# Kernel tuning notes

Measured on AMD Instinct MI355X. Metric: run time of the kernel, lower is better.

Reference implementation:

```python
import jax, jax.numpy as jnp
import numpy as np

N = 50000      # nodes
E = 800000     # edges
H, C = 4, 32   # heads, per-head channels
NF = 513       # n_fft//2 + 1 frequency bins
NMEL = 128
NEG_SLOPE_ATT = 0.2   # GATConv leaky_relu slope
NEG_SLOPE_MLP = 0.01  # F.leaky_relu default


def setup_inputs() -> dict:
    key = jax.random.key(0)
    ks = jax.random.split(key, 12)
    s = 0.05
    return {
        "x": jax.random.normal(ks[0], (N, NF), jnp.float32),
        "edge_index": jax.random.randint(ks[1], (2, E), 0, N, dtype=jnp.int32),
        "fb": jax.random.normal(ks[2], (NF, NMEL), jnp.float32) * s,
        "Wg": jax.random.normal(ks[3], (NMEL, H * C), jnp.float32) * s,
        "bias_g": jnp.zeros((H * C,), jnp.float32),
        "att_src": jax.random.normal(ks[4], (H, C), jnp.float32) * s,
        "att_dst": jax.random.normal(ks[5], (H, C), jnp.float32) * s,
        "W1": jax.random.normal(ks[6], (H * C, 256), jnp.float32) * s,
        "b1": jnp.zeros((256,), jnp.float32),
        "W2": jax.random.normal(ks[7], (256, 128), jnp.float32) * s,
        "b2": jnp.zeros((128,), jnp.float32),
        "W3": jax.random.normal(ks[8], (128, 10), jnp.float32) * s,
        "b3": jnp.zeros((10,), jnp.float32),
    }


def gat_conv(h, src, dst, att_src, att_dst, bias_g):
    # h: [N, H, C]; per-edge attention, segment softmax over dst, scatter-add
    a_s = jnp.einsum('nhc,hc->nh', h, att_src)  # [N, H]
    a_d = jnp.einsum('nhc,hc->nh', h, att_dst)  # [N, H]
    e = jax.nn.leaky_relu(a_s[src] + a_d[dst], NEG_SLOPE_ATT)  # [E', H]
    m = jax.ops.segment_max(e, dst, num_segments=N)            # [N, H]
    ex = jnp.exp(e - m[dst])
    denom = jax.ops.segment_sum(ex, dst, num_segments=N)       # [N, H]
    alpha = ex / denom[dst]                                    # [E', H]
    msg = h[src] * alpha[:, :, None]                           # [E', H, C]
    out = jax.ops.segment_sum(msg, dst, num_segments=N)        # [N, H, C]
    return out.reshape(N, H * C) + bias_g


def reference(x, edge_index, fb, Wg, bias_g, att_src, att_dst, W1, b1, W2, b2, W3, b3):
    # learnable mel filterbank projection: [N, NF] -> [N, NMEL]
    x = x @ fb
    # GATConv linear transform, split into heads
    h = (x @ Wg).reshape(N, H, C)
    # add self loops (PyG GATConv default add_self_loops=True)
    loop = jnp.arange(N, dtype=edge_index.dtype)
    src = jnp.concatenate([edge_index[0], loop])
    dst = jnp.concatenate([edge_index[1], loop])
    x = jax.nn.elu(gat_conv(h, src, dst, att_src, att_dst, bias_g))
    # dropout is identity in eval mode
    x = jax.nn.leaky_relu(x @ W1 + b1, NEG_SLOPE_MLP)
    x = jax.nn.leaky_relu(x @ W2 + b2, NEG_SLOPE_MLP)
    x = jax.nn.leaky_relu(x @ W3 + b3, NEG_SLOPE_MLP)
    return jax.nn.softmax(x, axis=-1)
```

## Files before the change

### kernel.cpp

```cpp
#include <hip/hip_runtime.h>
#include <hip/hip_bf16.h>

#define NN 50000
#define EE 800000
#define NFR 513
#define NMEL 128
#define HC 128

typedef __bf16 bf16x8 __attribute__((ext_vector_type(8)));
typedef float floatx4 __attribute__((ext_vector_type(4)));

__device__ __forceinline__ unsigned short f2b(float f) {
    unsigned u = __float_as_uint(f);
    u = (u + 0x7FFFu + ((u >> 16) & 1u)) >> 16;
    return (unsigned short)u;
}
__device__ __forceinline__ float b2f(unsigned short s) {
    return __uint_as_float(((unsigned)s) << 16);
}
__device__ __forceinline__ float lexp(float a) {
    a = a > 0.f ? a : 0.2f * a;
    return __expf(a);
}

__device__ __forceinline__ float ldf(const float* p, long i) { return p[i]; }
__device__ __forceinline__ void stf(float* p, long i, float v) { p[i] = v; }
__device__ __forceinline__ void stf(__hip_bfloat16* p, long i, float v) {
    ((unsigned short*)p)[i] = f2b(v);
}

#define BM 64
#define BN 64
#define BK 16

template<int EPI, typename TA, typename TB, typename TC>
__global__ __launch_bounds__(256) void gemm_k(const TA* __restrict__ A, const TB* __restrict__ B,
                                              TC* __restrict__ C, int M, int Nn, int K,
                                              const float* __restrict__ bias)
{
    __shared__ float As[BK][BM + 4];
    __shared__ float Bs[BK][BN + 4];
    const int t = threadIdx.x;
    const int row0 = blockIdx.x * BM;
    const int col0 = blockIdx.y * BN;
    const int tc = t & 15, tr = t >> 4;
    float acc[4][4] = {};

    for (int kb = 0; kb < K; kb += BK) {
        #pragma unroll
        for (int i = 0; i < 4; ++i) {
            int idx = i * 256 + t;
            int r = idx >> 4, k = idx & 15;
            int gr = row0 + r, gk = kb + k;
            float v = 0.f;
            if (gr < M && gk < K) v = ldf(A, (long)gr * K + gk);
            As[k][r] = v;
        }
        #pragma unroll
        for (int i = 0; i < 4; ++i) {
            int idx = i * 256 + t;
            int c = idx & 63, k = idx >> 6;
            int gk = kb + k, gc = col0 + c;
            float v = 0.f;
            if (gk < K && gc < Nn) v = ldf(B, (long)gk * Nn + gc);
            Bs[k][c] = v;
        }
        __syncthreads();
        #pragma unroll
        for (int kk = 0; kk < BK; ++kk) {
            float4 av = *reinterpret_cast<const float4*>(&As[kk][tr << 2]);
            float4 bv = *reinterpret_cast<const float4*>(&Bs[kk][tc << 2]);
            float a[4] = {av.x, av.y, av.z, av.w};
            float b[4] = {bv.x, bv.y, bv.z, bv.w};
            #pragma unroll
            for (int i = 0; i < 4; ++i)
                #pragma unroll
                for (int j = 0; j < 4; ++j)
                    acc[i][j] += a[i] * b[j];
        }
        __syncthreads();
    }

    #pragma unroll
    for (int i = 0; i < 4; ++i) {
        int gr = row0 + (tr << 2) + i;
        if (gr >= M) continue;
        #pragma unroll
        for (int j = 0; j < 4; ++j) {
            int gc = col0 + (tc << 2) + j;
            if (gc >= Nn) continue;
            float v = acc[i][j];
            if (EPI == 2) {
                stf(C, (long)gc * 544 + gr, v);
            } else {
                if (EPI == 1) { v += bias[gc]; v = v > 0.f ? v : 0.01f * v; }
                stf(C, (long)gr * Nn + gc, v);
            }
        }
    }
}

__global__ void k_trans(const float* __restrict__ in, __hip_bfloat16* __restrict__ outp,
                        int K, int N, int KP)
{
    int id = blockIdx.x * 256 + threadIdx.x;
    if (id >= N * KP) return;
    int n = id / KP, k = id % KP;
    float v = (k < K) ? in[(long)k * N + n] : 0.f;
    ((unsigned short*)outp)[id] = f2b(v);
}

#define PS 40

template<typename T> struct ARegs;
template<> struct ARegs<float> { float v[8]; };
template<> struct ARegs<__hip_bfloat16> { uint4 v; };

__device__ __forceinline__ void loadA_r(const float* __restrict__ A, ARegs<float>& r, int t,
                                        int row0, int M, int K, int kb)
{
    #pragma unroll
    for (int g = 0; g < 2; ++g) {
        int q = g * 256 + t;
        int row = q >> 3, k4 = (q & 7) * 4;
        int gr = row0 + row, gk = kb + k4;
        float f0 = 0.f, f1 = 0.f, f2 = 0.f, f3 = 0.f;
        if (gr < M) {
            const float* ap = A + (long)gr * K + gk;
            if (gk + 3 < K) {
                f0 = ap[0]; f1 = ap[1]; f2 = ap[2]; f3 = ap[3];
            } else {
                if (gk + 0 < K) f0 = ap[0];
                if (gk + 1 < K) f1 = ap[1];
                if (gk + 2 < K) f2 = ap[2];
            }
        }
        r.v[g * 4 + 0] = f0; r.v[g * 4 + 1] = f1;
        r.v[g * 4 + 2] = f2; r.v[g * 4 + 3] = f3;
    }
}

__device__ __forceinline__ void writeA_r(unsigned short* As, const ARegs<float>& r, int t)
{
    #pragma unroll
    for (int g = 0; g < 2; ++g) {
        int q = g * 256 + t;
        int row = q >> 3, k4 = (q & 7) * 4;
        ushort4 pk;
        pk.x = f2b(r.v[g * 4 + 0]); pk.y = f2b(r.v[g * 4 + 1]);
        pk.z = f2b(r.v[g * 4 + 2]); pk.w = f2b(r.v[g * 4 + 3]);
        *reinterpret_cast<ushort4*>(&As[row * PS + k4]) = pk;
    }
}

__device__ __forceinline__ void loadA_r(const __hip_bfloat16* __restrict__ A, ARegs<__hip_bfloat16>& r,
                                        int t, int row0, int M, int K, int kb)
{
    int row = t >> 2, k8 = (t & 3) * 8;
    int gr = row0 + row;
    uint4 val = make_uint4(0, 0, 0, 0);
    if (gr < M) val = *reinterpret_cast<const uint4*>(A + (long)gr * K + kb + k8);
    r.v = val;
}

__device__ __forceinline__ void writeA_r(unsigned short* As, const ARegs<__hip_bfloat16>& r, int t)
{
    int row = t >> 2, k8 = (t & 3) * 8;
    *reinterpret_cast<uint4*>(&As[row * PS + k8]) = r.v;
}

__device__ __forceinline__ void loadB_r(const __hip_bfloat16* __restrict__ Bt, uint4* bR, int t,
                                        int col0, int Nn, int KB, int kb)
{
    #pragma unroll
    for (int g = 0; g < 2; ++g) {
        int c = g * 256 + t;
        int row = c >> 2, k8 = (c & 3) * 8;
        int gn = col0 + row;
        uint4 val = make_uint4(0, 0, 0, 0);
        if (gn < Nn) val = *reinterpret_cast<const uint4*>(Bt + (long)gn * KB + kb + k8);
        bR[g] = val;
    }
}

__device__ __forceinline__ void writeB_r(unsigned short* Bs, const uint4* bR, int t)
{
    #pragma unroll
    for (int g = 0; g < 2; ++g) {
        int c = g * 256 + t;
        int row = c >> 2, k8 = (c & 3) * 8;
        *reinterpret_cast<uint4*>(&Bs[row * PS + k8]) = bR[g];
    }
}

template<int EPI, typename TA, typename TC>
__global__ __launch_bounds__(256) void mgemm(const TA* __restrict__ A,
                                             const __hip_bfloat16* __restrict__ Bt,
                                             TC* __restrict__ C,
                                             int M, int Nn, int K, int KB,
                                             const float* __restrict__ bias)
{
    __shared__ unsigned short As[2][64 * PS];
    __shared__ unsigned short Bs[2][128 * PS];
    const int t = threadIdx.x;
    const int row0 = blockIdx.x * 64;
    const int col0 = blockIdx.y * 128;
    const int wave = t >> 6, lane = t & 63;
    const int wm = (wave >> 1) * 32, wn = (wave & 1) * 64;
    const int lm = lane & 15, kq = lane >> 4;

    floatx4 acc[2][4];
    #pragma unroll
    for (int i = 0; i < 2; ++i)
        #pragma unroll
        for (int j = 0; j < 4; ++j)
            acc[i][j] = 0.f;

    ARegs<TA> aR;
    uint4 bR[2];
    loadA_r(A, aR, t, row0, M, K, 0);
    loadB_r(Bt, bR, t, col0, Nn, KB, 0);

    const int nIter = KB >> 5;
    int b = 0;
    for (int it = 0; it < nIter; ++it) {
        writeA_r(As[b], aR, t);
        writeB_r(Bs[b], bR, t);
        if (it + 1 < nIter) {
            loadA_r(A, aR, t, row0, M, K, (it + 1) * 32);
            loadB_r(Bt, bR, t, col0, Nn, KB, (it + 1) * 32);
        }
        asm volatile("s_waitcnt lgkmcnt(0)" ::: "memory");
        __builtin_amdgcn_s_barrier();
        __builtin_amdgcn_sched_barrier(0);

        bf16x8 af[2], bf[4];
        #pragma unroll
        for (int i = 0; i < 2; ++i)
            af[i] = *reinterpret_cast<const bf16x8*>(&As[b][(wm + i * 16 + lm) * PS + kq * 8]);
        #pragma unroll
        for (int j = 0; j < 4; ++j)
            bf[j] = *reinterpret_cast<const bf16x8*>(&Bs[b][(wn + j * 16 + lm) * PS + kq * 8]);
        #pragma unroll
        for (int i = 0; i < 2; ++i)
            #pragma unroll
            for (int j = 0; j < 4; ++j)
                acc[i][j] = __builtin_amdgcn_mfma_f32_16x16x32_bf16(af[i], bf[j], acc[i][j], 0, 0, 0);
        b ^= 1;
    }

    #pragma unroll
    for (int i = 0; i < 2; ++i) {
        #pragma unroll
        for (int r = 0; r < 4; ++r) {
            int gr = row0 + wm + i * 16 + kq * 4 + r;
            if (gr >= M) continue;
            #pragma unroll
            for (int j = 0; j < 4; ++j) {
                int gc = col0 + wn + j * 16 + lm;
                float v = acc[i][j][r];
                if (EPI == 1) { v += bias[gc]; v = v > 0.f ? v : 0.01f * v; }
                stf(C, (long)gr * Nn + gc, v);
            }
        }
    }
}

__global__ void k_att(const __hip_bfloat16* __restrict__ h, const float* __restrict__ att_src,
                      const float* __restrict__ att_dst,
                      float* __restrict__ a_s, float* __restrict__ a_d)
{
    int id = blockIdx.x * blockDim.x + threadIdx.x;
    if (id >= NN * 4) return;
    int n = id >> 2, hh = id & 3;
    const unsigned short* hr = (const unsigned short*)(h + (long)n * HC + hh * 32);
    float s1 = 0.f, s2 = 0.f;
    #pragma unroll
    for (int c = 0; c < 32; ++c) {
        float v = b2f(hr[c]);
        s1 += v * att_src[hh * 32 + c];
        s2 += v * att_dst[hh * 32 + c];
    }
    a_s[id] = s1;
    a_d[id] = s2;
}

__global__ void k_hist(const int* __restrict__ ei, int* __restrict__ hist)
{
    int e = blockIdx.x * 256 + threadIdx.x;
    if (e < EE) atomicAdd(&hist[ei[EE + e]], 1);
}

__global__ __launch_bounds__(512) void k_scan1(const int* __restrict__ hist, int* __restrict__ start,
                                               int* __restrict__ aux)
{
    __shared__ int sm[512];
    int t = threadIdx.x, i = blockIdx.x * 512 + t;
    int v = (i < NN) ? hist[i] : 0;
    sm[t] = v;
    __syncthreads();
    for (int off = 1; off < 512; off <<= 1) {
        int x = (t >= off) ? sm[t - off] : 0;
        __syncthreads();
        sm[t] += x;
        __syncthreads();
    }
    if (i < NN) start[i] = sm[t] - v;
    if (t == 511) aux[blockIdx.x] = sm[511];
}

__global__ void k_scan2(int* __restrict__ aux, int nb)
{
    if (blockIdx.x == 0 && threadIdx.x == 0) {
        int run = 0;
        for (int b = 0; b < nb; ++b) { int v = aux[b]; aux[b] = run; run += v; }
    }
}

__global__ __launch_bounds__(512) void k_scan3(int* __restrict__ start, int* __restrict__ cursor,
                                               const int* __restrict__ aux)
{
    int i = blockIdx.x * 512 + threadIdx.x;
    if (i < NN) {
        int v = start[i] + aux[blockIdx.x];
        start[i] = v;
        cursor[i] = v;
    }
    if (i == 0) start[NN] = EE;
}

__global__ void k_fill(const int* __restrict__ ei, int* __restrict__ cursor, int* __restrict__ sorted)
{
    int e = blockIdx.x * 256 + threadIdx.x;
    if (e >= EE) return;
    int s = ei[e], d = ei[EE + e];
    int pos = atomicAdd(&cursor[d], 1);
    sorted[pos] = s;
}

__global__ __launch_bounds__(256) void k_agg(const int* __restrict__ start, const int* __restrict__ sorted,
                                             const float* __restrict__ a_s, const float* __restrict__ a_d,
                                             const __hip_bfloat16* __restrict__ h,
                                             const float* __restrict__ bias_g,
                                             __hip_bfloat16* __restrict__ agg)
{
    int wave = threadIdx.x >> 6;
    int lane = threadIdx.x & 63;
    int d = blockIdx.x * 4 + wave;
    if (d >= NN) return;
    int hh = lane >> 4;
    float ad = a_d[d * 4 + hh];
    int e0 = start[d], e1 = start[d + 1];

    float ex = lexp(a_s[d * 4 + hh] + ad);
    unsigned hv = *reinterpret_cast<const unsigned*>(h + (long)d * HC + 2 * lane);
    float acc0 = ex * __uint_as_float(hv << 16);
    float acc1 = ex * __uint_as_float(hv & 0xffff0000u);
    float dsum = ex;

    int e = e0;
    for (; e + 4 <= e1; e += 4) {
        int s0 = sorted[e + 0], s1 = sorted[e + 1], s2 = sorted[e + 2], s3 = sorted[e + 3];
        float as0 = a_s[s0 * 4 + hh], as1 = a_s[s1 * 4 + hh];
        float as2 = a_s[s2 * 4 + hh], as3 = a_s[s3 * 4 + hh];
        unsigned h0 = *reinterpret_cast<const unsigned*>(h + (long)s0 * HC + 2 * lane);
        unsigned h1 = *reinterpret_cast<const unsigned*>(h + (long)s1 * HC + 2 * lane);
        unsigned h2 = *reinterpret_cast<const unsigned*>(h + (long)s2 * HC + 2 * lane);
        unsigned h3 = *reinterpret_cast<const unsigned*>(h + (long)s3 * HC + 2 * lane);
        float x0 = lexp(as0 + ad), x1 = lexp(as1 + ad), x2 = lexp(as2 + ad), x3 = lexp(as3 + ad);
        acc0 += x0 * __uint_as_float(h0 << 16);
        acc1 += x0 * __uint_as_float(h0 & 0xffff0000u);
        acc0 += x1 * __uint_as_float(h1 << 16);
        acc1 += x1 * __uint_as_float(h1 & 0xffff0000u);
        acc0 += x2 * __uint_as_float(h2 << 16);
        acc1 += x2 * __uint_as_float(h2 & 0xffff0000u);
        acc0 += x3 * __uint_as_float(h3 << 16);
        acc1 += x3 * __uint_as_float(h3 & 0xffff0000u);
        dsum += x0 + x1 + x2 + x3;
    }
    for (; e < e1; ++e) {
        int s = sorted[e];
        float xe = lexp(a_s[s * 4 + hh] + ad);
        unsigned hs = *reinterpret_cast<const unsigned*>(h + (long)s * HC + 2 * lane);
        acc0 += xe * __uint_as_float(hs << 16);
        acc1 += xe * __uint_as_float(hs & 0xffff0000u);
        dsum += xe;
    }

    float inv = 1.f / dsum;
    float2 bg = *reinterpret_cast<const float2*>(bias_g + 2 * lane);
    float v0 = acc0 * inv + bg.x;
    float v1 = acc1 * inv + bg.y;
    v0 = v0 > 0.f ? v0 : expm1f(v0);
    v1 = v1 > 0.f ? v1 : expm1f(v1);
    unsigned pk = (unsigned)f2b(v0) | ((unsigned)f2b(v1) << 16);
    *reinterpret_cast<unsigned*>((unsigned short*)agg + (long)d * HC + 2 * lane) = pk;
}

__global__ __launch_bounds__(256) void k_final(const __hip_bfloat16* __restrict__ x2, const float* __restrict__ W3,
                                               const float* __restrict__ b3, float* __restrict__ out)
{
    __shared__ float w3s[128 * 10];
    __shared__ float b3s[10];
    int t = threadIdx.x;
    for (int i = t; i < 128 * 10; i += 256) w3s[i] = W3[i];
    if (t < 10) b3s[t] = b3[t];
    __syncthreads();
    int n = blockIdx.x * 256 + t;
    if (n >= NN) return;

    float l[10];
    #pragma unroll
    for (int j = 0; j < 10; ++j) l[j] = b3s[j];
    const uint4* row = reinterpret_cast<const uint4*>(x2 + (long)n * 128);
    #pragma unroll 4
    for (int c8 = 0; c8 < 16; ++c8) {
        uint4 v = row[c8];
        const unsigned w[4] = {v.x, v.y, v.z, v.w};
        #pragma unroll
        for (int u = 0; u < 4; ++u) {
            float f0 = __uint_as_float(w[u] << 16);
            float f1 = __uint_as_float(w[u] & 0xffff0000u);
            const float* wr = &w3s[(c8 * 8 + u * 2) * 10];
            #pragma unroll
            for (int j = 0; j < 10; ++j) l[j] += f0 * wr[j] + f1 * wr[10 + j];
        }
    }
    float m = -1e30f;
    #pragma unroll
    for (int j = 0; j < 10; ++j) {
        float v = l[j];
        v = v > 0.f ? v : 0.01f * v;
        l[j] = v;
        m = fmaxf(m, v);
    }
    float sum = 0.f;
    #pragma unroll
    for (int j = 0; j < 10; ++j) { l[j] = __expf(l[j] - m); sum += l[j]; }
    float inv = 1.f / sum;
    #pragma unroll
    for (int j = 0; j < 10; ++j) out[(long)n * 10 + j] = l[j] * inv;
}

extern "C" void kernel_launch(void* const* d_in, const int* in_sizes, int n_in,
                              void* d_out, int out_size, void* d_ws, size_t ws_size,
                              hipStream_t stream)
{
    const float* x       = (const float*)d_in[0];
    const int*   ei      = (const int*)d_in[1];
    const float* fb      = (const float*)d_in[2];
    const float* Wg      = (const float*)d_in[3];
    const float* bias_g  = (const float*)d_in[4];
    const float* att_src = (const float*)d_in[5];
    const float* att_dst = (const float*)d_in[6];
    const float* W1      = (const float*)d_in[7];
    const float* b1      = (const float*)d_in[8];
    const float* W2      = (const float*)d_in[9];
    const float* b2      = (const float*)d_in[10];
    const float* W3      = (const float*)d_in[11];
    const float* b3      = (const float*)d_in[12];
    float* out = (float*)d_out;
    float* ws = (float*)d_ws;

    float* a_s = ws + 0;
    float* a_d = ws + 200000;
    __hip_bfloat16* fbWgT = (__hip_bfloat16*)(ws + 400000);
    __hip_bfloat16* W1T   = (__hip_bfloat16*)(ws + 434816);
    __hip_bfloat16* W2T   = (__hip_bfloat16*)(ws + 451200);
    int* hist   = (int*)(ws + 467584);
    int* startA = (int*)(ws + 517584);
    int* aux    = (int*)(ws + 567588);
    int* sorted = (int*)(ws + 567720);
    __hip_bfloat16* hbufB = (__hip_bfloat16*)(ws + 1367720);
    __hip_bfloat16* aggB  = (__hip_bfloat16*)(ws + 4567720);
    __hip_bfloat16* x1B   = (__hip_bfloat16*)(ws + 7767720);
    int* cursor = hist;
    __hip_bfloat16* x2B = hbufB;
    if (ws_size < (size_t)14167720 * sizeof(float)) return;

    hipMemsetAsync(ws + 400000, 0, (size_t)117584 * sizeof(float), stream);

    gemm_k<2, float, float, __hip_bfloat16><<<dim3(9, 2), 256, 0, stream>>>(fb, Wg, fbWgT, NFR, HC, NMEL, nullptr);
    k_trans<<<128, 256, 0, stream>>>(W1, W1T, 128, 256, 128);
    k_trans<<<128, 256, 0, stream>>>(W2, W2T, 256, 128, 256);

    mgemm<0, float, __hip_bfloat16><<<dim3(782, 1), 256, 0, stream>>>(x, fbWgT, hbufB, NN, HC, NFR, 544, nullptr);

    k_att<<<(NN * 4 + 255) / 256, 256, 0, stream>>>(hbufB, att_src, att_dst, a_s, a_d);

    k_hist<<<(EE + 255) / 256, 256, 0, stream>>>(ei, hist);
    k_scan1<<<98, 512, 0, stream>>>(hist, startA, aux);
    k_scan2<<<1, 64, 0, stream>>>(aux, 98);
    k_scan3<<<98, 512, 0, stream>>>(startA, cursor, aux);
    k_fill<<<(EE + 255) / 256, 256, 0, stream>>>(ei, cursor, sorted);

    k_agg<<<(NN + 3) / 4, 256, 0, stream>>>(startA, sorted, a_s, a_d, hbufB, bias_g, aggB);

    mgemm<1, __hip_bfloat16, __hip_bfloat16><<<dim3(782, 2), 256, 0, stream>>>(aggB, W1T, x1B, NN, 256, 128, 128, b1);

    mgemm<1, __hip_bfloat16, __hip_bfloat16><<<dim3(782, 1), 256, 0, stream>>>(x1B, W2T, x2B, NN, 128, 256, 256, b2);

    k_final<<<(NN + 255) / 256, 256, 0, stream>>>(x2B, W3, b3, out);
}
```

Before: 429.6 us.

## Add dedicated first GEMM keeping whole B tile in LDS and loading A directly

Replaces the generic double-buffered GEMM for the x @ (fb·Wg) projection with a specialised kernel of 512 threads and 128-row blocks. Half of the transposed B matrix is staged in shared memory per phase, while each wave reads its fp32 A rows straight from global memory into registers, converts them to bf16 and feeds MFMA without an LDS round trip for A. The odd 513th column is handled in a separate tail step. This aims to cut LDS traffic and barriers on the largest, memory-bound GEMM. The cost is uncoalesced per-lane strided A loads (8 consecutive floats per lane across rows) and a large shared allocation that limits occupancy.

Measured after the change: 450.1 us. 4.8% more time.

```diff
diff --git a/kernel.cpp b/kernel.cpp
--- a/kernel.cpp
+++ b/kernel.cpp
@@ -110,50 +110,84 @@
     ((unsigned short*)outp)[id] = f2b(v);
 }
 
+#define KC 32
+
+__global__ __launch_bounds__(512) void mgemm1(const float* __restrict__ A,
+                                              const __hip_bfloat16* __restrict__ Bt,
+                                              __hip_bfloat16* __restrict__ C)
+{
+    __shared__ unsigned short Bs[KC * 128 * 8];
+    const int t = threadIdx.x;
+    const unsigned short* BtU = (const unsigned short*)Bt;
+
+    const int wave = t >> 6, lane = t & 63;
+    const int lm = lane & 15, kq = lane >> 4;
+    const int row0g = blockIdx.x * 128 + wave * 16;
+
+    const int arow = row0g + lm;
+    const bool rv = arow < NN;
+    const float* ap = A + (long)arow * NFR;
+
+    floatx4 acc[8];
+    #pragma unroll
+    for (int j = 0; j < 8; ++j) acc[j] = 0.f;
+
+    for (int ph = 0; ph < 2; ++ph) {
+        __syncthreads();
+        #pragma unroll
+        for (int g = 0; g < 8; ++g) {
+            int i = g * 512 + t;
+            int col = i & 127, chunk = (i >> 7) + ph * KC;
+            *reinterpret_cast<uint4*>(&Bs[(size_t)i * 8]) =
+                *reinterpret_cast<const uint4*>(BtU + (size_t)col * 544 + chunk * 8);
+        }
+        __syncthreads();
+
+        #pragma unroll 4
+        for (int step = 0; step < 8; ++step) {
+            const int k0 = (ph * 8 + step) * 32 + kq * 8;
+            union { bf16x8 v; unsigned short u[8]; } af;
+            #pragma unroll
+            for (int i2 = 0; i2 < 8; ++i2) {
+                float fv = rv ? ap[k0 + i2] : 0.f;
+                af.u[i2] = f2b(fv);
+            }
+            const int chunk = step * 4 + kq;
+            #pragma unroll
+            for (int j = 0; j < 8; ++j) {
+                bf16x8 bf = *reinterpret_cast<const bf16x8*>(&Bs[((size_t)chunk * 128 + j * 16 + lm) * 8]);
+                acc[j] = __builtin_amdgcn_mfma_f32_16x16x32_bf16(af.v, bf, acc[j], 0, 0, 0);
+            }
+        }
+    }
+
+    {
+        union { bf16x8 v; unsigned short u[8]; } af;
+        #pragma unroll
+        for (int i2 = 0; i2 < 8; ++i2) af.u[i2] = 0;
+        if (kq == 0 && rv) af.u[0] = f2b(ap[512]);
+        #pragma unroll
+        for (int j = 0; j < 8; ++j) {
+            bf16x8 bf = *reinterpret_cast<const bf16x8*>(BtU + (size_t)(j * 16 + lm) * 544 + (64 + kq) * 8);
+            acc[j] = __builtin_amdgcn_mfma_f32_16x16x32_bf16(af.v, bf, acc[j], 0, 0, 0);
+        }
+    }
+
+    #pragma unroll
+    for (int r = 0; r < 4; ++r) {
+        int crow = row0g + kq * 4 + r;
+        if (crow >= NN) continue;
+        #pragma unroll
+        for (int j = 0; j < 8; ++j)
+            ((unsigned short*)C)[(long)crow * 128 + j * 16 + lm] = f2b(acc[j][r]);
+    }
+}
+
 #define PS 40
 
-template<typename T> struct ARegs;
-template<> struct ARegs<float> { float v[8]; };
-template<> struct ARegs<__hip_bfloat16> { uint4 v; };
-
-__device__ __forceinline__ void loadA_r(const float* __restrict__ A, ARegs<float>& r, int t,
-                                        int row0, int M, int K, int kb)
-{
-    #pragma unroll
-    for (int g = 0; g < 2; ++g) {
-        int q = g * 256 + t;
-        int row = q >> 3, k4 = (q & 7) * 4;
-        int gr = row0 + row, gk = kb + k4;
-        float f0 = 0.f, f1 = 0.f, f2 = 0.f, f3 = 0.f;
-        if (gr < M) {
-            const float* ap = A + (long)gr * K + gk;
-            if (gk + 3 < K) {
-                f0 = ap[0]; f1 = ap[1]; f2 = ap[2]; f3 = ap[3];
-            } else {
-                if (gk + 0 < K) f0 = ap[0];
-                if (gk + 1 < K) f1 = ap[1];
-                if (gk + 2 < K) f2 = ap[2];
-            }
-        }
-        r.v[g * 4 + 0] = f0; r.v[g * 4 + 1] = f1;
-        r.v[g * 4 + 2] = f2; r.v[g * 4 + 3] = f3;
-    }
-}
-
-__device__ __forceinline__ void writeA_r(unsigned short* As, const ARegs<float>& r, int t)
-{
-    #pragma unroll
-    for (int g = 0; g < 2; ++g) {
-        int q = g * 256 + t;
-        int row = q >> 3, k4 = (q & 7) * 4;
-        ushort4 pk;
-        pk.x = f2b(r.v[g * 4 + 0]); pk.y = f2b(r.v[g * 4 + 1]);
-        pk.z = f2b(r.v[g * 4 + 2]); pk.w = f2b(r.v[g * 4 + 3]);
-        *reinterpret_cast<ushort4*>(&As[row * PS + k4]) = pk;
-    }
-}
-
-__device__ __forceinline__ void loadA_r(const __hip_bfloat16* __restrict__ A, ARegs<__hip_bfloat16>& r,
+struct ARegsB { uint4 v; };
+
+__device__ __forceinline__ void loadA_r(const __hip_bfloat16* __restrict__ A, ARegsB& r,
                                         int t, int row0, int M, int K, int kb)
 {
     int row = t >> 2, k8 = (t & 3) * 8;
@@ -163,7 +197,7 @@
     r.v = val;
 }
 
-__device__ __forceinline__ void writeA_r(unsigned short* As, const ARegs<__hip_bfloat16>& r, int t)
+__device__ __forceinline__ void writeA_r(unsigned short* As, const ARegsB& r, int t)
 {
     int row = t >> 2, k8 = (t & 3) * 8;
     *reinterpret_cast<uint4*>(&As[row * PS + k8]) = r.v;
@@ -193,10 +227,10 @@
     }
 }
 
-template<int EPI, typename TA, typename TC>
-__global__ __launch_bounds__(256) void mgemm(const TA* __restrict__ A,
+template<int EPI>
+__global__ __launch_bounds__(256) void mgemm(const __hip_bfloat16* __restrict__ A,
                                              const __hip_bfloat16* __restrict__ Bt,
-                                             TC* __restrict__ C,
+                                             __hip_bfloat16* __restrict__ C,
                                              int M, int Nn, int K, int KB,
                                              const float* __restrict__ bias)
 {
@@ -216,7 +250,7 @@
         for (int j = 0; j < 4; ++j)
             acc[i][j] = 0.f;
 
-    ARegs<TA> aR;
+    ARegsB aR;
     uint4 bR[2];
     loadA_r(A, aR, t, row0, M, K, 0);
     loadB_r(Bt, bR, t, col0, Nn, KB, 0);
@@ -484,7 +518,7 @@
     k_trans<<<128, 256, 0, stream>>>(W1, W1T, 128, 256, 128);
     k_trans<<<128, 256, 0, stream>>>(W2, W2T, 256, 128, 256);
 
-    mgemm<0, float, __hip_bfloat16><<<dim3(782, 1), 256, 0, stream>>>(x, fbWgT, hbufB, NN, HC, NFR, 544, nullptr);
+    mgemm1<<<391, 512, 0, stream>>>(x, fbWgT, hbufB);
 
     k_att<<<(NN * 4 + 255) / 256, 256, 0, stream>>>(hbufB, att_src, att_dst, a_s, a_d);
 
@@ -496,9 +530,9 @@
 
     k_agg<<<(NN + 3) / 4, 256, 0, stream>>>(startA, sorted, a_s, a_d, hbufB, bias_g, aggB);
 
-    mgemm<1, __hip_bfloat16, __hip_bfloat16><<<dim3(782, 2), 256, 0, stream>>>(aggB, W1T, x1B, NN, 256, 128, 128, b1);
-
-    mgemm<1, __hip_bfloat16, __hip_bfloat16><<<dim3(782, 1), 256, 0, stream>>>(x1B, W2T, x2B, NN, 128, 256, 256, b2);
+    mgemm<1><<<dim3(782, 2), 256, 0, stream>>>(aggB, W1T, x1B, NN, 256, 128, 128, b1);
+
+    mgemm<1><<<dim3(782, 1), 256, 0, stream>>>(x1B, W2T, x2B, NN, 128, 256, 256, b2);
 
     k_final<<<(NN + 255) / 256, 256, 0, stream>>>(x2B, W3, b3, out);
 }
```
